# Performance work log

Hardware: AMD Instinct MI355X
Metric: run time of the kernel (lower is better)

## Reference

```python
import jax, jax.numpy as jnp
import numpy as np

D = 512      # dim_model
F = 2048     # dim_feedforward
E = 8        # num_experts
K = 2        # num_experts_per_token
B, S = 2, 4096


def setup_inputs() -> dict:
    key = jax.random.key(0)
    ks = jax.random.split(key, 8)
    sd = 1.0 / np.sqrt(D)
    sf = 1.0 / np.sqrt(F)
    return {
        "x": jax.random.normal(ks[0], (B, S, D), dtype=jnp.float32),
        "router_w": jax.random.uniform(ks[1], (D, E), jnp.float32, -sd, sd),
        "router_b": jax.random.uniform(ks[2], (E,), jnp.float32, -sd, sd),
        "w1": jax.random.uniform(ks[3], (E, D, F), jnp.float32, -sd, sd),
        "b1": jax.random.uniform(ks[4], (E, F), jnp.float32, -sd, sd),
        "w2": jax.random.uniform(ks[5], (E, F, D), jnp.float32, -sf, sf),
        "b2": jax.random.uniform(ks[6], (E, D), jnp.float32, -sf, sf),
    }


def reference(x, router_w, router_b, w1, b1, w2, b2):
    orig_shape = x.shape
    flat = x.reshape(-1, orig_shape[-1])                     # [T, D]
    logits = flat @ router_w + router_b                      # [T, E]
    gates = jax.nn.softmax(logits, axis=-1)                  # [T, E]
    top_vals, top_idx = jax.lax.top_k(gates, K)              # [T, K]
    top_vals = top_vals / jnp.sum(top_vals, axis=-1, keepdims=True)
    # combine weight per (token, expert): zero for unselected experts,
    # so dense per-expert evaluation yields identical math to masked dispatch.
    onehot = jax.nn.one_hot(top_idx, E, dtype=flat.dtype)    # [T, K, E]
    comb = jnp.einsum('tk,tke->te', top_vals, onehot)        # [T, E]
    # expert FFNs over all tokens (dropout is identity in eval)
    hidden = jax.nn.relu(jnp.einsum('td,edf->etf', flat, w1) + b1[:, None, :])  # [E, T, F]
    eout = jnp.einsum('etf,efd->etd', hidden, w2) + b2[:, None, :]              # [E, T, D]
    out = jnp.einsum('te,etd->td', comb, eout)               # [T, D]
    return out.reshape(orig_shape)
```

## Files before the change

kernel.cpp:

```cpp
#include <hip/hip_runtime.h>
#include <cstdint>
#include <cstddef>

#define TD 512
#define TF 2048
#define NE 8
#define NT 8192
#define CAP 17408

using u16 = unsigned short;
using u32 = unsigned int;

typedef __attribute__((ext_vector_type(8))) __bf16 bf16x8;
typedef __attribute__((ext_vector_type(4))) float f32x4;

__device__ __forceinline__ u16 f2bf(float f) {
  u32 u = __float_as_uint(f);
  u32 r = (u + 0x7fffu + ((u >> 16) & 1u)) >> 16;
  return (u16)r;
}

__device__ __forceinline__ void load_lds16(const void* g, void* l) {
  __builtin_amdgcn_global_load_lds(
      (const __attribute__((address_space(1))) void*)g,
      (__attribute__((address_space(3))) void*)l, 16, 0, 0);
}

__global__ void zero_kernel(float* __restrict__ out) {
  int i = blockIdx.x * 256 + threadIdx.x;
  float4 z = make_float4(0.f, 0.f, 0.f, 0.f);
  *reinterpret_cast<float4*>(out + (size_t)i * 4) = z;
}

__global__ void transpose_cvt_kernel(const float* __restrict__ in, u16* __restrict__ out,
                                     int R, int C) {
  __shared__ u16 tile[32][33];
  int c0 = blockIdx.x * 32, r0 = blockIdx.y * 32;
  const float* ib = in + (size_t)blockIdx.z * R * C;
  u16* ob = out + (size_t)blockIdx.z * R * C;
  #pragma unroll
  for (int rr = 0; rr < 32; rr += 8) {
    int r = r0 + threadIdx.y + rr;
    int c = c0 + threadIdx.x;
    tile[threadIdx.y + rr][threadIdx.x] = f2bf(ib[(size_t)r * C + c]);
  }
  __syncthreads();
  #pragma unroll
  for (int rr = 0; rr < 32; rr += 8) {
    int oc = c0 + threadIdx.y + rr;
    int orr = r0 + threadIdx.x;
    ob[(size_t)oc * R + orr] = tile[threadIdx.x][threadIdx.y + rr];
  }
}

__global__ void router_kernel(const float* __restrict__ x, const float* __restrict__ rw,
                              const float* __restrict__ rb, int2* __restrict__ tokE,
                              float2* __restrict__ tokG, u16* __restrict__ xb) {
  int wv = threadIdx.x >> 6;
  int lane = threadIdx.x & 63;
  int t = blockIdx.x * 4 + wv;
  const float* xr = x + (size_t)t * TD;
  float4 a0 = *reinterpret_cast<const float4*>(xr + lane * 4);
  float4 a1 = *reinterpret_cast<const float4*>(xr + 256 + lane * 4);
  {
    u16 o[8];
    o[0] = f2bf(a0.x); o[1] = f2bf(a0.y); o[2] = f2bf(a0.z); o[3] = f2bf(a0.w);
    o[4] = f2bf(a1.x); o[5] = f2bf(a1.y); o[6] = f2bf(a1.z); o[7] = f2bf(a1.w);
    u16* xo = xb + (size_t)t * TD;
    *reinterpret_cast<uint2*>(xo + lane * 4) = *reinterpret_cast<uint2*>(o);
    *reinterpret_cast<uint2*>(xo + 256 + lane * 4) = *reinterpret_cast<uint2*>(o + 4);
  }
  float p[NE];
  #pragma unroll
  for (int e = 0; e < NE; e++) p[e] = 0.f;
  float av[8] = {a0.x, a0.y, a0.z, a0.w, a1.x, a1.y, a1.z, a1.w};
  #pragma unroll
  for (int j = 0; j < 8; j++) {
    int d = (j < 4) ? (lane * 4 + j) : (256 + lane * 4 + j - 4);
    const float* r = rw + (size_t)d * NE;
    #pragma unroll
    for (int e = 0; e < NE; e++) p[e] += av[j] * r[e];
  }
  #pragma unroll
  for (int off = 32; off >= 1; off >>= 1) {
    #pragma unroll
    for (int e = 0; e < NE; e++) p[e] += __shfl_xor(p[e], off);
  }
  if (lane == 0) {
    float l[NE];
    #pragma unroll
    for (int e = 0; e < NE; e++) l[e] = p[e] + rb[e];
    float m = l[0];
    #pragma unroll
    for (int e = 1; e < NE; e++) m = fmaxf(m, l[e]);
    float g[NE];
    #pragma unroll
    for (int e = 0; e < NE; e++) g[e] = __expf(l[e] - m);
    int i0 = 0;
    #pragma unroll
    for (int e = 1; e < NE; e++) if (g[e] > g[i0]) i0 = e;
    int i1 = -1;
    #pragma unroll
    for (int e = 0; e < NE; e++) {
      if (e == i0) continue;
      if (i1 < 0 || g[e] > g[i1]) i1 = e;
    }
    float inv = 1.f / (g[i0] + g[i1]);
    tokE[t] = make_int2(i0, i1);
    tokG[t] = make_float2(g[i0] * inv, g[i1] * inv);
  }
}

__global__ void count_offsets_kernel(const int2* __restrict__ tokE, int* __restrict__ offs,
                                     int* __restrict__ cursors) {
  __shared__ int hist[NE];
  if (threadIdx.x < NE) {
    hist[threadIdx.x] = 0;
    cursors[threadIdx.x * 16] = 0;
  }
  __syncthreads();
  for (int t = threadIdx.x; t < NT; t += 1024) {
    int2 e = tokE[t];
    atomicAdd(&hist[e.x], 1);
    atomicAdd(&hist[e.y], 1);
  }
  __syncthreads();
  if (threadIdx.x == 0) {
    int tot = 0;
    for (int e = 0; e < NE; e++) {
      offs[e] = tot;
      tot += (hist[e] + 127) & ~127;
    }
    offs[NE] = tot;
  }
}

__global__ void fill_kernel(const int* __restrict__ offs, int* __restrict__ tok,
                            float* __restrict__ gate, int* __restrict__ sexp) {
  int s = blockIdx.x * 256 + threadIdx.x;
  int e = NE - 1;
  #pragma unroll
  for (int i = 0; i < NE; i++)
    if (s >= offs[i] && s < offs[i + 1]) e = i;
  sexp[s] = e;
  tok[s] = -1;
  gate[s] = 0.f;
}

__global__ void scatter_kernel(const int2* __restrict__ tokE, const float2* __restrict__ tokG,
                               const int* __restrict__ offs, int* __restrict__ cursors,
                               int* __restrict__ tok, float* __restrict__ gate) {
  int t = blockIdx.x * 256 + threadIdx.x;
  int lane = threadIdx.x & 63;
  int2 e = tokE[t];
  float2 g = tokG[t];
  #pragma unroll
  for (int k = 0; k < 2; k++) {
    int ek = k ? e.y : e.x;
    float gk = k ? g.y : g.x;
    #pragma unroll
    for (int ex = 0; ex < NE; ex++) {
      unsigned long long mask = __ballot(ek == ex);
      if (ek == ex) {
        int leader = __ffsll(mask) - 1;
        int rank = __popcll(mask & ((1ull << lane) - 1ull));
        int base = 0;
        if (lane == leader) base = atomicAdd(&cursors[ex * 16], __popcll(mask));
        base = __shfl(base, leader);
        int s = offs[ex] + base + rank;
        tok[s] = t;
        gate[s] = gk;
      }
    }
  }
}

__global__ __launch_bounds__(256, 2) void gemm1_kernel(
    const u16* __restrict__ xb, const u16* __restrict__ w1t,
    const float* __restrict__ b1, const int* __restrict__ tok,
    const int* __restrict__ sexp, u16* __restrict__ H) {
  __shared__ u16 As[128 * 64];
  __shared__ u16 Bs[128 * 64];
  __shared__ int tokS[128];
  const int tid = threadIdx.x;
  const int s0 = blockIdx.x * 128;
  const int f0 = blockIdx.y * 128;
  const int e = sexp[s0];
  if (tid < 128) {
    int t = tok[s0 + tid];
    tokS[tid] = t < 0 ? 0 : t;
  }
  __syncthreads();

  const int lane = tid & 63;
  const int wv = tid >> 6;
  const int srow = lane >> 3;
  const int scol = (lane & 7) * 8;
  const int wm = (wv >> 1) * 64;
  const int wn = (wv & 1) * 64;
  const int mrow = lane & 15;
  const int koff = (lane >> 4) * 8;

  f32x4 zero = {0.f, 0.f, 0.f, 0.f};
  f32x4 acc[4][4];
  #pragma unroll
  for (int i = 0; i < 4; i++)
    #pragma unroll
    for (int j = 0; j < 4; j++) acc[i][j] = zero;

  const u16* bbase = w1t + ((size_t)e * TF + f0) * TD;

  for (int k0 = 0; k0 < TD; k0 += 64) {
    if (k0) __syncthreads();
    #pragma unroll
    for (int p = 0; p < 4; p++) {
      int row = wv * 32 + p * 8 + srow;
      load_lds16(xb + (size_t)tokS[row] * TD + k0 + scol, &As[(wv * 32 + p * 8) * 64]);
      load_lds16(bbase + (size_t)row * TD + k0 + scol, &Bs[(wv * 32 + p * 8) * 64]);
    }
    __syncthreads();
    #pragma unroll
    for (int ks = 0; ks < 2; ks++) {
      bf16x8 a[4], b[4];
      #pragma unroll
      for (int i = 0; i < 4; i++)
        a[i] = *reinterpret_cast<const bf16x8*>(&As[(wm + i * 16 + mrow) * 64 + ks * 32 + koff]);
      #pragma unroll
      for (int j = 0; j < 4; j++)
        b[j] = *reinterpret_cast<const bf16x8*>(&Bs[(wn + j * 16 + mrow) * 64 + ks * 32 + koff]);
      #pragma unroll
      for (int i = 0; i < 4; i++)
        #pragma unroll
        for (int j = 0; j < 4; j++)
          acc[i][j] = __builtin_amdgcn_mfma_f32_16x16x32_bf16(a[i], b[j], acc[i][j], 0, 0, 0);
    }
  }

  const int quad = lane >> 4;
  float bv[4];
  #pragma unroll
  for (int j = 0; j < 4; j++) bv[j] = b1[e * TF + f0 + wn + j * 16 + mrow];
  #pragma unroll
  for (int i = 0; i < 4; i++) {
    #pragma unroll
    for (int r = 0; r < 4; r++) {
      int row = s0 + wm + i * 16 + quad * 4 + r;
      u16* hrow = H + (size_t)row * TF + f0;
      #pragma unroll
      for (int j = 0; j < 4; j++) {
        float v = acc[i][j][r] + bv[j];
        v = v > 0.f ? v : 0.f;
        hrow[wn + j * 16 + mrow] = f2bf(v);
      }
    }
  }
}

__global__ __launch_bounds__(256, 2) void gemm2_kernel(
    const u16* __restrict__ H, const u16* __restrict__ w2t,
    const float* __restrict__ b2, const int* __restrict__ tok,
    const float* __restrict__ gate, const int* __restrict__ sexp,
    float* __restrict__ out) {
  __shared__ u16 As[128 * 64];
  __shared__ u16 Bs[128 * 64];
  __shared__ int tokS[128];
  __shared__ float gateS[128];
  const int tid = threadIdx.x;
  const int s0 = blockIdx.x * 128;
  const int d0 = blockIdx.y * 128;
  const int e = sexp[s0];
  if (tid < 128) {
    tokS[tid] = tok[s0 + tid];
    gateS[tid] = gate[s0 + tid];
  }
  __syncthreads();

  const int lane = tid & 63;
  const int wv = tid >> 6;
  const int srow = lane >> 3;
  const int scol = (lane & 7) * 8;
  const int wm = (wv >> 1) * 64;
  const int wn = (wv & 1) * 64;
  const int mrow = lane & 15;
  const int koff = (lane >> 4) * 8;

  f32x4 zero = {0.f, 0.f, 0.f, 0.f};
  f32x4 acc[4][4];
  #pragma unroll
  for (int i = 0; i < 4; i++)
    #pragma unroll
    for (int j = 0; j < 4; j++) acc[i][j] = zero;

  const u16* bbase = w2t + ((size_t)e * TD + d0) * TF;

  for (int k0 = 0; k0 < TF; k0 += 64) {
    if (k0) __syncthreads();
    #pragma unroll
    for (int p = 0; p < 4; p++) {
      int row = wv * 32 + p * 8 + srow;
      load_lds16(H + (size_t)(s0 + row) * TF + k0 + scol, &As[(wv * 32 + p * 8) * 64]);
      load_lds16(bbase + (size_t)row * TF + k0 + scol, &Bs[(wv * 32 + p * 8) * 64]);
    }
    __syncthreads();
    #pragma unroll
    for (int ks = 0; ks < 2; ks++) {
      bf16x8 a[4], b[4];
      #pragma unroll
      for (int i = 0; i < 4; i++)
        a[i] = *reinterpret_cast<const bf16x8*>(&As[(wm + i * 16 + mrow) * 64 + ks * 32 + koff]);
      #pragma unroll
      for (int j = 0; j < 4; j++)
        b[j] = *reinterpret_cast<const bf16x8*>(&Bs[(wn + j * 16 + mrow) * 64 + ks * 32 + koff]);
      #pragma unroll
      for (int i = 0; i < 4; i++)
        #pragma unroll
        for (int j = 0; j < 4; j++)
          acc[i][j] = __builtin_amdgcn_mfma_f32_16x16x32_bf16(a[i], b[j], acc[i][j], 0, 0, 0);
    }
  }

  const int quad = lane >> 4;
  float bv[4];
  #pragma unroll
  for (int j = 0; j < 4; j++) bv[j] = b2[e * TD + d0 + wn + j * 16 + mrow];
  #pragma unroll
  for (int i = 0; i < 4; i++) {
    #pragma unroll
    for (int r = 0; r < 4; r++) {
      int rl = wm + i * 16 + quad * 4 + r;
      int t = tokS[rl];
      if (t < 0) continue;
      float g = gateS[rl];
      float* orow = out + (size_t)t * TD + d0;
      #pragma unroll
      for (int j = 0; j < 4; j++) {
        atomicAdd(&orow[wn + j * 16 + mrow], g * (acc[i][j][r] + bv[j]));
      }
    }
  }
}

extern "C" void kernel_launch(void* const* d_in, const int* in_sizes, int n_in,
                              void* d_out, int out_size, void* d_ws, size_t ws_size,
                              hipStream_t stream) {
  const float* x  = (const float*)d_in[0];
  const float* rw = (const float*)d_in[1];
  const float* rb = (const float*)d_in[2];
  const float* w1 = (const float*)d_in[3];
  const float* b1 = (const float*)d_in[4];
  const float* w2 = (const float*)d_in[5];
  const float* b2 = (const float*)d_in[6];
  float* out = (float*)d_out;

  char* w = (char*)d_ws;
  u16* xb   = (u16*)w;            w += (size_t)NT * TD * 2;
  u16* w1t  = (u16*)w;            w += (size_t)NE * TD * TF * 2;
  u16* w2t  = (u16*)w;            w += (size_t)NE * TF * TD * 2;
  u16* H    = (u16*)w;            w += (size_t)CAP * TF * 2;
  int* tok  = (int*)w;            w += (size_t)CAP * 4;
  float* gate = (float*)w;        w += (size_t)CAP * 4;
  int* sexp = (int*)w;            w += (size_t)CAP * 4;
  int2* tokE = (int2*)w;          w += (size_t)NT * 8;
  float2* tokG = (float2*)w;      w += (size_t)NT * 8;
  int* cursors = (int*)w;         w += 1024;
  int* offs = (int*)w;            w += 256;

  zero_kernel<<<dim3((NT * TD) / (256 * 4)), dim3(256), 0, stream>>>(out);
  transpose_cvt_kernel<<<dim3(TF / 32, TD / 32, NE), dim3(32, 8), 0, stream>>>(w1, w1t, TD, TF);
  transpose_cvt_kernel<<<dim3(TD / 32, TF / 32, NE), dim3(32, 8), 0, stream>>>(w2, w2t, TF, TD);
  router_kernel<<<dim3(NT / 4), dim3(256), 0, stream>>>(x, rw, rb, tokE, tokG, xb);
  count_offsets_kernel<<<dim3(1), dim3(1024), 0, stream>>>(tokE, offs, cursors);
  fill_kernel<<<dim3(CAP / 256), dim3(256), 0, stream>>>(offs, tok, gate, sexp);
  scatter_kernel<<<dim3(NT / 256), dim3(256), 0, stream>>>(tokE, tokG, offs, cursors, tok, gate);
  gemm1_kernel<<<dim3(CAP / 128, TF / 128), dim3(256), 0, stream>>>(xb, w1t, b1, tok, sexp, H);
  gemm2_kernel<<<dim3(CAP / 128, TD / 128), dim3(256), 0, stream>>>(H, w2t, b2, tok, gate, sexp, out);
}
```

Before: 304.5 us.

## Swizzle LDS tiles, split-K gemm2, and raise occupancy bounds

Applies an XOR swizzle to the 16-byte column chunks when staging A/B tiles into LDS and uses the matching swizzled read addresses, to reduce LDS bank conflicts on the MFMA operand loads. The second GEMM is split along K into two halves over a new grid z dimension, with the bias added only by the first half and both halves accumulating through atomics. This doubles gemm2's block count, since it otherwise has few blocks. Launch bounds are raised to 4 blocks per CU for both GEMMs, which may force register limits or spills, and the split doubles the atomic traffic to the output.

```diff
diff --git a/kernel.cpp b/kernel.cpp
--- a/kernel.cpp
+++ b/kernel.cpp
@@ -175,7 +175,7 @@
   }
 }
 
-__global__ __launch_bounds__(256, 2) void gemm1_kernel(
+__global__ __launch_bounds__(256, 4) void gemm1_kernel(
     const u16* __restrict__ xb, const u16* __restrict__ w1t,
     const float* __restrict__ b1, const int* __restrict__ tok,
     const int* __restrict__ sexp, u16* __restrict__ H) {
@@ -195,11 +195,12 @@
   const int lane = tid & 63;
   const int wv = tid >> 6;
   const int srow = lane >> 3;
-  const int scol = (lane & 7) * 8;
+  const int scol = (((lane & 7) ^ srow) & 7) * 8;
   const int wm = (wv >> 1) * 64;
   const int wn = (wv & 1) * 64;
   const int mrow = lane & 15;
-  const int koff = (lane >> 4) * 8;
+  const int quad = lane >> 4;
+  const int rq = mrow & 7;
 
   f32x4 zero = {0.f, 0.f, 0.f, 0.f};
   f32x4 acc[4][4];
@@ -224,10 +225,12 @@
       bf16x8 a[4], b[4];
       #pragma unroll
       for (int i = 0; i < 4; i++)
-        a[i] = *reinterpret_cast<const bf16x8*>(&As[(wm + i * 16 + mrow) * 64 + ks * 32 + koff]);
+        a[i] = *reinterpret_cast<const bf16x8*>(
+            &As[(wm + i * 16 + mrow) * 64 + ((ks * 4 + quad) ^ rq) * 8]);
       #pragma unroll
       for (int j = 0; j < 4; j++)
-        b[j] = *reinterpret_cast<const bf16x8*>(&Bs[(wn + j * 16 + mrow) * 64 + ks * 32 + koff]);
+        b[j] = *reinterpret_cast<const bf16x8*>(
+            &Bs[(wn + j * 16 + mrow) * 64 + ((ks * 4 + quad) ^ rq) * 8]);
       #pragma unroll
       for (int i = 0; i < 4; i++)
         #pragma unroll
@@ -236,7 +239,6 @@
     }
   }
 
-  const int quad = lane >> 4;
   float bv[4];
   #pragma unroll
   for (int j = 0; j < 4; j++) bv[j] = b1[e * TF + f0 + wn + j * 16 + mrow];
@@ -256,7 +258,7 @@
   }
 }
 
-__global__ __launch_bounds__(256, 2) void gemm2_kernel(
+__global__ __launch_bounds__(256, 4) void gemm2_kernel(
     const u16* __restrict__ H, const u16* __restrict__ w2t,
     const float* __restrict__ b2, const int* __restrict__ tok,
     const float* __restrict__ gate, const int* __restrict__ sexp,
@@ -268,6 +270,7 @@
   const int tid = threadIdx.x;
   const int s0 = blockIdx.x * 128;
   const int d0 = blockIdx.y * 128;
+  const int kz = blockIdx.z;
   const int e = sexp[s0];
   if (tid < 128) {
     tokS[tid] = tok[s0 + tid];
@@ -278,11 +281,12 @@
   const int lane = tid & 63;
   const int wv = tid >> 6;
   const int srow = lane >> 3;
-  const int scol = (lane & 7) * 8;
+  const int scol = (((lane & 7) ^ srow) & 7) * 8;
   const int wm = (wv >> 1) * 64;
   const int wn = (wv & 1) * 64;
   const int mrow = lane & 15;
-  const int koff = (lane >> 4) * 8;
+  const int quad = lane >> 4;
+  const int rq = mrow & 7;
 
   f32x4 zero = {0.f, 0.f, 0.f, 0.f};
   f32x4 acc[4][4];
@@ -292,9 +296,11 @@
     for (int j = 0; j < 4; j++) acc[i][j] = zero;
 
   const u16* bbase = w2t + ((size_t)e * TD + d0) * TF;
-
-  for (int k0 = 0; k0 < TF; k0 += 64) {
-    if (k0) __syncthreads();
+  const int kbeg = kz * (TF / 2);
+  const int kend = kbeg + (TF / 2);
+
+  for (int k0 = kbeg; k0 < kend; k0 += 64) {
+    if (k0 != kbeg) __syncthreads();
     #pragma unroll
     for (int p = 0; p < 4; p++) {
       int row = wv * 32 + p * 8 + srow;
@@ -307,10 +313,12 @@
       bf16x8 a[4], b[4];
       #pragma unroll
       for (int i = 0; i < 4; i++)
-        a[i] = *reinterpret_cast<const bf16x8*>(&As[(wm + i * 16 + mrow) * 64 + ks * 32 + koff]);
+        a[i] = *reinterpret_cast<const bf16x8*>(
+            &As[(wm + i * 16 + mrow) * 64 + ((ks * 4 + quad) ^ rq) * 8]);
       #pragma unroll
       for (int j = 0; j < 4; j++)
-        b[j] = *reinterpret_cast<const bf16x8*>(&Bs[(wn + j * 16 + mrow) * 64 + ks * 32 + koff]);
+        b[j] = *reinterpret_cast<const bf16x8*>(
+            &Bs[(wn + j * 16 + mrow) * 64 + ((ks * 4 + quad) ^ rq) * 8]);
       #pragma unroll
       for (int i = 0; i < 4; i++)
         #pragma unroll
@@ -319,10 +327,10 @@
     }
   }
 
-  const int quad = lane >> 4;
   float bv[4];
   #pragma unroll
-  for (int j = 0; j < 4; j++) bv[j] = b2[e * TD + d0 + wn + j * 16 + mrow];
+  for (int j = 0; j < 4; j++)
+    bv[j] = (kz == 0) ? b2[e * TD + d0 + wn + j * 16 + mrow] : 0.f;
   #pragma unroll
   for (int i = 0; i < 4; i++) {
     #pragma unroll
@@ -373,5 +381,5 @@
   fill_kernel<<<dim3(CAP / 256), dim3(256), 0, stream>>>(offs, tok, gate, sexp);
   scatter_kernel<<<dim3(NT / 256), dim3(256), 0, stream>>>(tokE, tokG, offs, cursors, tok, gate);
   gemm1_kernel<<<dim3(CAP / 128, TF / 128), dim3(256), 0, stream>>>(xb, w1t, b1, tok, sexp, H);
-  gemm2_kernel<<<dim3(CAP / 128, TD / 128), dim3(256), 0, stream>>>(H, w2t, b2, tok, gate, sexp, out);
-}
+  gemm2_kernel<<<dim3(CAP / 128, TD / 128, 2), dim3(256), 0, stream>>>(H, w2t, b2, tok, gate, sexp, out);
+}
```

After: 326.2 us. 7.1% more time.
